# Kernel tuning notes

Measured on AMD Instinct MI355X. Metric: run time of the kernel, lower is better.

## Reference

```python
import jax, jax.numpy as jnp
import numpy as np

N_NODES = 100000
N_HEDGES = 20000
N_PAIRS = 1600000
D = 128


def setup_inputs() -> dict:
    key = jax.random.key(0)
    k1, k2, k3, k4, k5 = jax.random.split(key, 5)
    features = jax.random.normal(k1, (N_NODES, D), dtype=jnp.float32)
    W = jax.random.normal(k2, (D, D), dtype=jnp.float32) * (1.0 / np.sqrt(D))
    b = jax.random.normal(k3, (D,), dtype=jnp.float32) * 0.01
    node_idx = jax.random.randint(k4, (N_PAIRS,), 0, N_NODES, dtype=jnp.int32)
    hedge_idx = jax.random.randint(k5, (N_PAIRS,), 0, N_HEDGES, dtype=jnp.int32)
    return {"features": features, "W": W, "b": b,
            "node_idx": node_idx, "hedge_idx": hedge_idx, "n_hedges": N_HEDGES}


def reference(features, W, b, node_idx, hedge_idx, n_hedges):
    # features: [N, D]; (node_idx, hedge_idx): [E] incidence pairs
    N = features.shape[0]
    ones = jnp.ones(node_idx.shape, dtype=features.dtype)
    # node -> hyperedge mean (DGL copy_u + mean over 'in' etype)
    deg_e = jax.ops.segment_sum(ones, hedge_idx, num_segments=n_hedges)  # [He]
    h_edge = jax.ops.segment_sum(features[node_idx], hedge_idx, num_segments=n_hedges)
    h_edge = h_edge / jnp.maximum(deg_e, 1.0)[:, None]  # zero-degree edges -> 0
    # hyperedge -> node mean (copy_u + mean over 'contains' etype)
    deg_n = jax.ops.segment_sum(ones, node_idx, num_segments=N)  # [N]
    h_node = jax.ops.segment_sum(h_edge[hedge_idx], node_idx, num_segments=N)
    h_node = h_node / jnp.maximum(deg_n, 1.0)[:, None]
    # nn.Linear: x @ W.T + b
    return h_node @ W.T + b
```

## Files before the change

### kernel.cpp

```cpp
#include <hip/hip_runtime.h>

static constexpr int kD = 128;
static constexpr int kHedges = 20000;

static constexpr int kNCE = 157;
static constexpr int kCapCE = 11264;
static constexpr int kNCN = 196;
static constexpr int kCapCN = 9216;
static constexpr int kSliceE = 896;
static constexpr int kSliceN = 768;

__device__ __forceinline__ float u2f(unsigned u) { return __uint_as_float(u); }
__device__ __forceinline__ unsigned f2u(float f) { return __float_as_uint(f); }

__device__ __forceinline__ unsigned bfpack(float x, float y) {
  unsigned ux = f2u(x); ux = (ux + 0x7FFFu + ((ux >> 16) & 1u)) >> 16;
  unsigned uy = f2u(y); uy = (uy + 0x7FFFu + ((uy >> 16) & 1u)) & 0xFFFF0000u;
  return ux | uy;
}
__device__ __forceinline__ void bf8_acc(uint4 v, float* a) {
  a[0] += u2f(v.x << 16); a[1] += u2f(v.x & 0xFFFF0000u);
  a[2] += u2f(v.y << 16); a[3] += u2f(v.y & 0xFFFF0000u);
  a[4] += u2f(v.z << 16); a[5] += u2f(v.z & 0xFFFF0000u);
  a[6] += u2f(v.w << 16); a[7] += u2f(v.w & 0xFFFF0000u);
}

__global__ __launch_bounds__(256) void partition_coarse(
    const float* __restrict__ feat, unsigned* __restrict__ feat_bf, int n_feat,
    const int* __restrict__ node_idx, const int* __restrict__ hedge_idx,
    int n_pairs,
    int* __restrict__ gcnt_e, int* __restrict__ buf_e,
    int* __restrict__ gcnt_n, int* __restrict__ buf_n) {
  __shared__ int hist_e[kNCE], base_e[kNCE], hist_n[kNCN], base_n[kNCN];
  const int tid = threadIdx.x;
  {
    const int n8 = n_feat >> 3;
    for (int t = blockIdx.x * 256 + tid; t < n8; t += gridDim.x * 256) {
      long long i = (long long)t * 8;
      const float4 v0 = *(const float4*)(feat + i);
      const float4 v1 = *(const float4*)(feat + i + 4);
      uint4 o;
      o.x = bfpack(v0.x, v0.y); o.y = bfpack(v0.z, v0.w);
      o.z = bfpack(v1.x, v1.y); o.w = bfpack(v1.z, v1.w);
      *(uint4*)(feat_bf + (i >> 1)) = o;
    }
  }
  const int per_block = (n_pairs + gridDim.x - 1) / gridDim.x;
  const int s = blockIdx.x * per_block;
  const int e = min(s + per_block, n_pairs);
  for (int i = tid; i < kNCE; i += 256) hist_e[i] = 0;
  for (int i = tid; i < kNCN; i += 256) hist_n[i] = 0;
  __syncthreads();
  for (int i = s + tid; i < e; i += 256) {
    atomicAdd(&hist_e[hedge_idx[i] >> 7], 1);
    atomicAdd(&hist_n[node_idx[i] >> 9], 1);
  }
  __syncthreads();
  for (int i = tid; i < kNCE; i += 256) {
    int h = hist_e[i];
    base_e[i] = (h > 0) ? atomicAdd(&gcnt_e[i], h) : 0;
    hist_e[i] = 0;
  }
  for (int i = tid; i < kNCN; i += 256) {
    int h = hist_n[i];
    base_n[i] = (h > 0) ? atomicAdd(&gcnt_n[i], h) : 0;
    hist_n[i] = 0;
  }
  __syncthreads();
  for (int i = s + tid; i < e; i += 256) {
    int n = node_idx[i], h = hedge_idx[i];
    int be = h >> 7;
    int pe = base_e[be] + atomicAdd(&hist_e[be], 1);
    if (pe < kCapCE) buf_e[(long long)be * kCapCE + pe] = (n << 7) | (h & 127);
    int bn = n >> 9;
    int pn = base_n[bn] + atomicAdd(&hist_n[bn], 1);
    if (pn < kCapCN) buf_n[(long long)bn * kCapCN + pn] = (h << 9) | (n & 511);
  }
}

__global__ __launch_bounds__(512) void subsort_kernel(
    int* __restrict__ buf_e, const int* __restrict__ gcnt_e, int* __restrict__ seg_e,
    int* __restrict__ buf_n, const int* __restrict__ gcnt_n, int* __restrict__ seg_n) {
  __shared__ int sbuf[kCapCE];
  __shared__ int bins[513];
  __shared__ int cur[512];
  __shared__ int segs[513];
  __shared__ int wtot[8];
  const int tid = threadIdx.x;
  int nbins, shift, cnt; int* src; int* segout;
  if (blockIdx.x < kNCE) {
    int cb = blockIdx.x; nbins = 128; shift = 7;
    src = buf_e + (long long)cb * kCapCE;
    cnt = min(gcnt_e[cb], kCapCE);
    segout = seg_e + cb * 129;
  } else {
    int cb = blockIdx.x - kNCE; nbins = 512; shift = 9;
    src = buf_n + (long long)cb * kCapCN;
    cnt = min(gcnt_n[cb], kCapCN);
    segout = seg_n + cb * 513;
  }
  const int mask = nbins - 1;
  for (int i = tid; i < nbins; i += 512) bins[i] = 0;
  __syncthreads();
  for (int i = tid; i < cnt; i += 512) atomicAdd(&bins[src[i] & mask], 1);
  __syncthreads();
  const int lane = tid & 63, wid = tid >> 6;
  int v = (tid < nbins) ? bins[tid] : 0;
  int x = v;
#pragma unroll
  for (int d = 1; d < 64; d <<= 1) {
    int y = __shfl_up(x, d, 64);
    if (lane >= d) x += y;
  }
  if (lane == 63) wtot[wid] = x;
  __syncthreads();
  int add = 0;
  for (int w = 0; w < wid; ++w) add += wtot[w];
  if (tid < nbins) { segs[tid + 1] = x + add; cur[tid] = x + add - v; }
  if (tid == 0) segs[0] = 0;
  __syncthreads();
  for (int i = tid; i < cnt; i += 512) {
    int p = src[i];
    int r = atomicAdd(&cur[p & mask], 1);
    sbuf[r] = p >> shift;
  }
  __syncthreads();
  for (int i = tid; i < cnt; i += 512) src[i] = sbuf[i];
  for (int j = tid; j <= nbins; j += 512) segout[j] = segs[j];
}

__global__ __launch_bounds__(128) void gather_edge_v2(
    const unsigned* __restrict__ feat_bf, const int* __restrict__ buf_e,
    const int* __restrict__ seg_e, unsigned* __restrict__ h_edge, int n_hedges) {
  __shared__ int ebuf[kSliceE];
  __shared__ int segl[9];
  const int b = blockIdx.x;
  const int tid = threadIdx.x;
  const int h0 = b * 8;
  const int cb = h0 >> 7, j0 = h0 & 127;
  if (tid < 9) segl[tid] = seg_e[cb * 129 + j0 + tid];
  __syncthreads();
  const int sbase = segl[0];
  const int n_sl = min(segl[8] - sbase, kSliceE);
  const int* src = buf_e + (long long)cb * kCapCE + sbase;
  for (int i = tid; i < n_sl; i += 128) ebuf[i] = src[i];
  __syncthreads();
  const int g = tid >> 4, lane = tid & 15, cw = lane * 4;
  int gh = h0 + g;
  if (gh >= n_hedges) return;
  const int deg = segl[g + 1] - segl[g];
  const int s0 = min(segl[g] - sbase, n_sl);
  const int e0 = min(segl[g + 1] - sbase, n_sl);
  float a[8] = {}, a2[8] = {};
  int j = s0;
  for (; j + 7 < e0; j += 8) {
    uint4 v0 = *(const uint4*)(feat_bf + (long long)ebuf[j] * 64 + cw);
    uint4 v1 = *(const uint4*)(feat_bf + (long long)ebuf[j + 1] * 64 + cw);
    uint4 v2 = *(const uint4*)(feat_bf + (long long)ebuf[j + 2] * 64 + cw);
    uint4 v3 = *(const uint4*)(feat_bf + (long long)ebuf[j + 3] * 64 + cw);
    uint4 v4 = *(const uint4*)(feat_bf + (long long)ebuf[j + 4] * 64 + cw);
    uint4 v5 = *(const uint4*)(feat_bf + (long long)ebuf[j + 5] * 64 + cw);
    uint4 v6 = *(const uint4*)(feat_bf + (long long)ebuf[j + 6] * 64 + cw);
    uint4 v7 = *(const uint4*)(feat_bf + (long long)ebuf[j + 7] * 64 + cw);
    bf8_acc(v0, a); bf8_acc(v1, a2); bf8_acc(v2, a); bf8_acc(v3, a2);
    bf8_acc(v4, a); bf8_acc(v5, a2); bf8_acc(v6, a); bf8_acc(v7, a2);
  }
  for (; j < e0; ++j) {
    uint4 v = *(const uint4*)(feat_bf + (long long)ebuf[j] * 64 + cw);
    bf8_acc(v, a);
  }
#pragma unroll
  for (int t = 0; t < 8; ++t) a[t] += a2[t];
  float inv = 1.0f / fmaxf((float)deg, 1.0f);
  uint4 o;
  o.x = bfpack(a[0] * inv, a[1] * inv);
  o.y = bfpack(a[2] * inv, a[3] * inv);
  o.z = bfpack(a[4] * inv, a[5] * inv);
  o.w = bfpack(a[6] * inv, a[7] * inv);
  *(uint4*)(h_edge + (long long)gh * 64 + cw) = o;
}

static constexpr int kWRow = 68;
__global__ __launch_bounds__(256) void edge_linear_v4(
    unsigned* __restrict__ h_edge, const float* __restrict__ W, int n_rows) {
  __shared__ unsigned Wt2[kD * kWRow];
  __shared__ float hT[kD * 64];
  const int tid = threadIdx.x;
  const int row0 = blockIdx.x * 64;
  for (int i = tid; i < kD * 64; i += 256) {
    int k = i & 127, j = i >> 7;
    float c0 = W[(2 * j) * kD + k];
    float c1 = W[(2 * j + 1) * kD + k];
    Wt2[k * kWRow + j] = bfpack(c0, c1);
  }
  {
    const int r = tid & 63, o = tid >> 6;
    const uint4* hp = (const uint4*)(h_edge + (long long)(row0 + r) * 64 + o * 16);
#pragma unroll
    for (int q = 0; q < 4; ++q) {
      uint4 v = hp[q];
      int k0 = o * 32 + q * 8;
      hT[(k0 + 0) * 64 + r] = u2f(v.x << 16);
      hT[(k0 + 1) * 64 + r] = u2f(v.x & 0xFFFF0000u);
      hT[(k0 + 2) * 64 + r] = u2f(v.y << 16);
      hT[(k0 + 3) * 64 + r] = u2f(v.y & 0xFFFF0000u);
      hT[(k0 + 4) * 64 + r] = u2f(v.z << 16);
      hT[(k0 + 5) * 64 + r] = u2f(v.z & 0xFFFF0000u);
      hT[(k0 + 6) * 64 + r] = u2f(v.w << 16);
      hT[(k0 + 7) * 64 + r] = u2f(v.w & 0xFFFF0000u);
    }
  }
  __syncthreads();
  const int c8 = tid & 15;
  const int rg = tid >> 4;
  float4 acc[4][2] = {};
#pragma unroll 2
  for (int k = 0; k < kD; ++k) {
    const uint4 wp = *(const uint4*)(&Wt2[k * kWRow + c8 * 4]);
    const float4 h4 = *(const float4*)(&hT[k * 64 + rg * 4]);
    const float w0 = u2f(wp.x << 16), w1 = u2f(wp.x & 0xFFFF0000u);
    const float w2 = u2f(wp.y << 16), w3 = u2f(wp.y & 0xFFFF0000u);
    const float w4 = u2f(wp.z << 16), w5 = u2f(wp.z & 0xFFFF0000u);
    const float w6 = u2f(wp.w << 16), w7 = u2f(wp.w & 0xFFFF0000u);
    const float hh[4] = {h4.x, h4.y, h4.z, h4.w};
#pragma unroll
    for (int i = 0; i < 4; ++i) {
      acc[i][0].x = fmaf(hh[i], w0, acc[i][0].x);
      acc[i][0].y = fmaf(hh[i], w1, acc[i][0].y);
      acc[i][0].z = fmaf(hh[i], w2, acc[i][0].z);
      acc[i][0].w = fmaf(hh[i], w3, acc[i][0].w);
      acc[i][1].x = fmaf(hh[i], w4, acc[i][1].x);
      acc[i][1].y = fmaf(hh[i], w5, acc[i][1].y);
      acc[i][1].z = fmaf(hh[i], w6, acc[i][1].z);
      acc[i][1].w = fmaf(hh[i], w7, acc[i][1].w);
    }
  }
  long long rr = row0 + rg * 4;
#pragma unroll
  for (int i = 0; i < 4; ++i) {
    uint4 o;
    o.x = bfpack(acc[i][0].x, acc[i][0].y);
    o.y = bfpack(acc[i][0].z, acc[i][0].w);
    o.z = bfpack(acc[i][1].x, acc[i][1].y);
    o.w = bfpack(acc[i][1].z, acc[i][1].w);
    *(uint4*)(h_edge + (rr + i) * 64 + c8 * 4) = o;
  }
}

__global__ __launch_bounds__(128) void gather_node_v2(
    const unsigned* __restrict__ t_edge, const int* __restrict__ buf_n,
    const int* __restrict__ seg_n, const float* __restrict__ bias,
    float* __restrict__ out, int n_nodes) {
  __shared__ int ebuf[kSliceN];
  __shared__ int segl[33];
  const int b = blockIdx.x;
  const int tid = threadIdx.x;
  const int n0 = b * 32;
  const int cb = n0 >> 9, j0 = n0 & 511;
  if (tid < 33) segl[tid] = seg_n[cb * 513 + j0 + tid];
  __syncthreads();
  const int sbase = segl[0];
  const int n_sl = min(segl[32] - sbase, kSliceN);
  const int* src = buf_n + (long long)cb * kCapCN + sbase;
  for (int i = tid; i < n_sl; i += 128) ebuf[i] = src[i];
  __syncthreads();
  const int g = tid >> 4, lane = tid & 15, cw = lane * 4;
  const float4 b0 = *(const float4*)(bias + lane * 8);
  const float4 b1 = *(const float4*)(bias + lane * 8 + 4);
  for (int nl = g; nl < 32; nl += 8) {
    int gn = n0 + nl;
    if (gn >= n_nodes) continue;
    const int deg = segl[nl + 1] - segl[nl];
    const int s0 = min(segl[nl] - sbase, n_sl);
    const int e0 = min(segl[nl + 1] - sbase, n_sl);
    float a[8] = {}, a2[8] = {};
    int j = s0;
    for (; j + 7 < e0; j += 8) {
      uint4 v0 = *(const uint4*)(t_edge + (long long)ebuf[j] * 64 + cw);
      uint4 v1 = *(const uint4*)(t_edge + (long long)ebuf[j + 1] * 64 + cw);
      uint4 v2 = *(const uint4*)(t_edge + (long long)ebuf[j + 2] * 64 + cw);
      uint4 v3 = *(const uint4*)(t_edge + (long long)ebuf[j + 3] * 64 + cw);
      uint4 v4 = *(const uint4*)(t_edge + (long long)ebuf[j + 4] * 64 + cw);
      uint4 v5 = *(const uint4*)(t_edge + (long long)ebuf[j + 5] * 64 + cw);
      uint4 v6 = *(const uint4*)(t_edge + (long long)ebuf[j + 6] * 64 + cw);
      uint4 v7 = *(const uint4*)(t_edge + (long long)ebuf[j + 7] * 64 + cw);
      bf8_acc(v0, a); bf8_acc(v1, a2); bf8_acc(v2, a); bf8_acc(v3, a2);
      bf8_acc(v4, a); bf8_acc(v5, a2); bf8_acc(v6, a); bf8_acc(v7, a2);
    }
    for (; j < e0; ++j) {
      uint4 v = *(const uint4*)(t_edge + (long long)ebuf[j] * 64 + cw);
      bf8_acc(v, a);
    }
#pragma unroll
    for (int t = 0; t < 8; ++t) a[t] += a2[t];
    float inv = 1.0f / fmaxf((float)deg, 1.0f);
    float4 o0, o1;
    o0.x = fmaf(a[0], inv, b0.x); o0.y = fmaf(a[1], inv, b0.y);
    o0.z = fmaf(a[2], inv, b0.z); o0.w = fmaf(a[3], inv, b0.w);
    o1.x = fmaf(a[4], inv, b1.x); o1.y = fmaf(a[5], inv, b1.y);
    o1.z = fmaf(a[6], inv, b1.z); o1.w = fmaf(a[7], inv, b1.w);
    float* op = out + (long long)gn * kD + lane * 8;
    *(float4*)op = o0;
    *(float4*)(op + 4) = o1;
  }
}

extern "C" void kernel_launch(void* const* d_in, const int* in_sizes, int n_in,
                              void* d_out, int out_size, void* d_ws, size_t ws_size,
                              hipStream_t stream) {
  const float* feat      = (const float*)d_in[0];
  const float* W         = (const float*)d_in[1];
  const float* b         = (const float*)d_in[2];
  const int*   node_idx  = (const int*)d_in[3];
  const int*   hedge_idx = (const int*)d_in[4];

  const int n_pairs  = in_sizes[3];
  const int n_nodes  = in_sizes[0] / kD;
  const int n_hedges = kHedges;
  const int n_feat   = in_sizes[0];

  unsigned* feat_bf = (unsigned*)d_out;

  const int n_rows_pad = ((n_hedges + 63) / 64) * 64;
  unsigned* h_edge = (unsigned*)d_ws;
  int* buf_e = (int*)(h_edge + (size_t)n_rows_pad * 64);
  int* buf_n = buf_e + (size_t)kNCE * kCapCE;
  int* seg_e = buf_n + (size_t)kNCN * kCapCN;
  int* seg_n = seg_e + (size_t)kNCE * 129;
  int* gcnt_e = seg_n + (size_t)kNCN * 513;
  int* gcnt_n = gcnt_e + kNCE;

  hipMemsetAsync(gcnt_e, 0, (size_t)(kNCE + kNCN) * sizeof(int), stream);

  partition_coarse<<<512, 256, 0, stream>>>(
      feat, feat_bf, n_feat,
      node_idx, hedge_idx, n_pairs, gcnt_e, buf_e, gcnt_n, buf_n);

  subsort_kernel<<<kNCE + kNCN, 512, 0, stream>>>(
      buf_e, gcnt_e, seg_e, buf_n, gcnt_n, seg_n);

  gather_edge_v2<<<(n_hedges + 7) / 8, 128, 0, stream>>>(
      feat_bf, buf_e, seg_e, h_edge, n_hedges);

  edge_linear_v4<<<n_rows_pad / 64, 256, 0, stream>>>(h_edge, W, n_rows_pad);

  gather_node_v2<<<(n_nodes + 31) / 32, 128, 0, stream>>>(
      h_edge, buf_n, seg_n, b, (float*)d_out, n_nodes);
}
```

Before: 285.9 us.

## Stage partitioned pairs in shared memory before coalesced bucket scatter

The coarse partition kernel now computes per-block bucket offsets with a wave prefix scan and first scatters each pair into a locally bucket-sorted shared-memory buffer. It then writes runs out to global buckets contiguously, so the global stores are coalesced rather than random. The grid grows so each block handles at most 3200 pairs, which fits the shared buffer. This adds shared-memory use and extra syncs, and it caps per-block work, which raises the number of global atomics on the bucket counters.

```diff
diff --git a/kernel.cpp b/kernel.cpp
--- a/kernel.cpp
+++ b/kernel.cpp
@@ -9,6 +9,7 @@
 static constexpr int kCapCN = 9216;
 static constexpr int kSliceE = 896;
 static constexpr int kSliceN = 768;
+static constexpr int kPmax = 3200;
 
 __device__ __forceinline__ float u2f(unsigned u) { return __uint_as_float(u); }
 __device__ __forceinline__ unsigned f2u(float f) { return __float_as_uint(f); }
@@ -31,7 +32,11 @@
     int n_pairs,
     int* __restrict__ gcnt_e, int* __restrict__ buf_e,
     int* __restrict__ gcnt_n, int* __restrict__ buf_n) {
-  __shared__ int hist_e[kNCE], base_e[kNCE], hist_n[kNCN], base_n[kNCN];
+  __shared__ unsigned lbuf_e[kPmax];
+  __shared__ unsigned lbuf_n[kPmax];
+  __shared__ int he[kNCE], se[kNCE];
+  __shared__ int hn[kNCN], sn_[kNCN];
+  __shared__ int wtot[4];
   const int tid = threadIdx.x;
   {
     const int n8 = n_feat >> 3;
@@ -48,33 +53,82 @@
   const int per_block = (n_pairs + gridDim.x - 1) / gridDim.x;
   const int s = blockIdx.x * per_block;
   const int e = min(s + per_block, n_pairs);
-  for (int i = tid; i < kNCE; i += 256) hist_e[i] = 0;
-  for (int i = tid; i < kNCN; i += 256) hist_n[i] = 0;
+  const int cnt = max(e - s, 0);
+  for (int i = tid; i < kNCE; i += 256) he[i] = 0;
+  for (int i = tid; i < kNCN; i += 256) hn[i] = 0;
   __syncthreads();
   for (int i = s + tid; i < e; i += 256) {
-    atomicAdd(&hist_e[hedge_idx[i] >> 7], 1);
-    atomicAdd(&hist_n[node_idx[i] >> 9], 1);
-  }
-  __syncthreads();
-  for (int i = tid; i < kNCE; i += 256) {
-    int h = hist_e[i];
-    base_e[i] = (h > 0) ? atomicAdd(&gcnt_e[i], h) : 0;
-    hist_e[i] = 0;
-  }
-  for (int i = tid; i < kNCN; i += 256) {
-    int h = hist_n[i];
-    base_n[i] = (h > 0) ? atomicAdd(&gcnt_n[i], h) : 0;
-    hist_n[i] = 0;
+    atomicAdd(&he[hedge_idx[i] >> 7], 1);
+    atomicAdd(&hn[node_idx[i] >> 9], 1);
+  }
+  __syncthreads();
+  const int lane = tid & 63, wid = tid >> 6;
+  {
+    int v = (tid < kNCE) ? he[tid] : 0;
+    int x = v;
+#pragma unroll
+    for (int d = 1; d < 64; d <<= 1) {
+      int y = __shfl_up(x, d, 64);
+      if (lane >= d) x += y;
+    }
+    if (lane == 63) wtot[wid] = x;
+    __syncthreads();
+    int add = 0;
+    for (int w = 0; w < wid; ++w) add += wtot[w];
+    if (tid < kNCE) {
+      int lofs = x + add - v;
+      int base = (v > 0) ? atomicAdd(&gcnt_e[tid], v) : 0;
+      se[tid] = base - lofs;
+      he[tid] = lofs;
+    }
+  }
+  __syncthreads();
+  {
+    int v = (tid < kNCN) ? hn[tid] : 0;
+    int x = v;
+#pragma unroll
+    for (int d = 1; d < 64; d <<= 1) {
+      int y = __shfl_up(x, d, 64);
+      if (lane >= d) x += y;
+    }
+    if (lane == 63) wtot[wid] = x;
+    __syncthreads();
+    int add = 0;
+    for (int w = 0; w < wid; ++w) add += wtot[w];
+    if (tid < kNCN) {
+      int lofs = x + add - v;
+      int base = (v > 0) ? atomicAdd(&gcnt_n[tid], v) : 0;
+      sn_[tid] = base - lofs;
+      hn[tid] = lofs;
+    }
   }
   __syncthreads();
   for (int i = s + tid; i < e; i += 256) {
-    int n = node_idx[i], h = hedge_idx[i];
-    int be = h >> 7;
-    int pe = base_e[be] + atomicAdd(&hist_e[be], 1);
-    if (pe < kCapCE) buf_e[(long long)be * kCapCE + pe] = (n << 7) | (h & 127);
-    int bn = n >> 9;
-    int pn = base_n[bn] + atomicAdd(&hist_n[bn], 1);
-    if (pn < kCapCN) buf_n[(long long)bn * kCapCN + pn] = (h << 9) | (n & 511);
+    const unsigned n = (unsigned)node_idx[i];
+    const unsigned h = (unsigned)hedge_idx[i];
+    const int be = (int)(h >> 7);
+    const int p = atomicAdd(&he[be], 1);
+    lbuf_e[p] = (n << 15) | h;
+    const int bn = (int)(n >> 9);
+    const int q = atomicAdd(&hn[bn], 1);
+    lbuf_n[q] = (h << 17) | n;
+  }
+  __syncthreads();
+  for (int i = tid; i < cnt; i += 256) {
+    const unsigned v = lbuf_e[i];
+    const int h = (int)(v & 0x7FFFu);
+    const int n = (int)(v >> 15);
+    const int b = h >> 7;
+    const int pe = se[b] + i;
+    if (pe < kCapCE) buf_e[(long long)b * kCapCE + pe] = (n << 7) | (h & 127);
+  }
+  for (int i = tid; i < cnt; i += 256) {
+    const unsigned v = lbuf_n[i];
+    const int n = (int)(v & 0x1FFFFu);
+    const int h = (int)(v >> 17);
+    const int b = n >> 9;
+    const int pn = sn_[b] + i;
+    if (pn < kCapCN) buf_n[(long long)b * kCapCN + pn] = (h << 9) | (n & 511);
   }
 }
 
@@ -332,7 +386,10 @@
 
   hipMemsetAsync(gcnt_e, 0, (size_t)(kNCE + kNCN) * sizeof(int), stream);
 
-  partition_coarse<<<512, 256, 0, stream>>>(
+  int pgrid = (n_pairs + kPmax - 1) / kPmax;
+  if (pgrid < 512) pgrid = 512;
+
+  partition_coarse<<<pgrid, 256, 0, stream>>>(
       feat, feat_bf, n_feat,
       node_idx, hedge_idx, n_pairs, gcnt_e, buf_e, gcnt_n, buf_n);
 
```

New measurement: 277.2 us. 1.03x faster.
